# Optimization experiments

Hardware: AMD Instinct MI355X
Metric: run time of the kernel (lower is better)

## Reference

```python
import jax, jax.numpy as jnp
import numpy as np

# Swin block config (matches init_kwargs)
DIM = 192
HEADS = 6
HEAD_DIM = 32
INNER = HEADS * HEAD_DIM  # 192
MLP = 768
WS = 7                    # window size
DISP = WS // 2            # cyclic shift displacement = 3
NEG = -1e9                # stands in for -inf in the shift masks
EPS = 1e-5


def setup_inputs() -> dict:
    key = jax.random.key(0)
    ks = jax.random.split(key, 8)
    B, H, W = 8, 112, 112
    x = jax.random.normal(ks[0], (B, H, W, DIM), dtype=jnp.float32)
    w_qkv = jax.random.normal(ks[1], (DIM, 3 * INNER), dtype=jnp.float32) * 0.02
    w_out = jax.random.normal(ks[2], (INNER, DIM), dtype=jnp.float32) * 0.02
    b_out = jnp.zeros((DIM,), jnp.float32)
    pos_emb = jax.random.normal(ks[3], (2 * WS - 1, 2 * WS - 1), dtype=jnp.float32)
    ln1_g = jnp.ones((DIM,), jnp.float32)
    ln1_b = jnp.zeros((DIM,), jnp.float32)
    ln2_g = jnp.ones((DIM,), jnp.float32)
    ln2_b = jnp.zeros((DIM,), jnp.float32)
    w1 = jax.random.normal(ks[4], (DIM, MLP), dtype=jnp.float32) * 0.02
    b1 = jnp.zeros((MLP,), jnp.float32)
    w2 = jax.random.normal(ks[5], (MLP, DIM), dtype=jnp.float32) * 0.02
    b2 = jnp.zeros((DIM,), jnp.float32)
    return {"x": x, "w_qkv": w_qkv, "w_out": w_out, "b_out": b_out,
            "pos_emb": pos_emb, "ln1_g": ln1_g, "ln1_b": ln1_b,
            "ln2_g": ln2_g, "ln2_b": ln2_b,
            "w1": w1, "b1": b1, "w2": w2, "b2": b2}


def _layernorm(x, g, b):
    mu = jnp.mean(x, axis=-1, keepdims=True)
    var = jnp.var(x, axis=-1, keepdims=True)
    return (x - mu) * jax.lax.rsqrt(var + EPS) * g + b


def _rel_bias(pos_emb):
    # relative position bias, gathered to (ws^2, ws^2)
    coords = jnp.stack(jnp.meshgrid(jnp.arange(WS), jnp.arange(WS), indexing="ij"), -1).reshape(-1, 2)
    rel = coords[:, None, :] - coords[None, :, :] + WS - 1  # in [0, 2*WS-2]
    return pos_emb[rel[..., 0], rel[..., 1]]


def _shift_masks(nw_h, nw_w):
    ws2 = WS * WS
    ul = jnp.zeros((ws2, ws2), jnp.float32)
    ul = ul.at[-DISP * WS:, :-DISP * WS].set(NEG)
    ul = ul.at[:-DISP * WS, -DISP * WS:].set(NEG)
    lr = jnp.zeros((WS, WS, WS, WS), jnp.float32)
    lr = lr.at[:, -DISP:, :, :-DISP].set(NEG)
    lr = lr.at[:, :-DISP:, :, -DISP:].set(NEG)
    lr = lr.reshape(ws2, ws2)
    full = jnp.zeros((nw_h * nw_w, ws2, ws2), jnp.float32)
    full = full.at[-nw_w:].add(ul)            # bottom row of windows
    full = full.at[nw_w - 1::nw_w].add(lr)    # rightmost column of windows
    return full


def _window_attention(x, w_qkv, w_out, b_out, pos_emb):
    x = jnp.roll(x, (-DISP, -DISP), axis=(1, 2))  # cyclic shift
    B, H, W, _ = x.shape
    nw_h, nw_w = H // WS, W // WS
    ws2 = WS * WS
    qkv = x @ w_qkv  # (B,H,W,3*INNER)
    qkv = qkv.reshape(B, nw_h, WS, nw_w, WS, 3, HEADS, HEAD_DIM)
    # -> (3, B, heads, n_windows, ws^2, head_dim)
    qkv = qkv.transpose(5, 0, 6, 1, 3, 2, 4, 7).reshape(3, B, HEADS, nw_h * nw_w, ws2, HEAD_DIM)
    q, k, v = qkv[0], qkv[1], qkv[2]
    dots = jnp.einsum("bhwid,bhwjd->bhwij", q, k) * (HEAD_DIM ** -0.5)
    dots = dots + _rel_bias(pos_emb)                       # (ws2,ws2) broadcast
    dots = dots + _shift_masks(nw_h, nw_w)                 # (nw,ws2,ws2) broadcast
    attn = jax.nn.softmax(dots, axis=-1)
    out = jnp.einsum("bhwij,bhwjd->bhwid", attn, v)
    # merge windows back: (B, nw_h, WS, nw_w, WS, heads*head_dim)
    out = out.reshape(B, HEADS, nw_h, nw_w, WS, WS, HEAD_DIM)
    out = out.transpose(0, 2, 4, 3, 5, 1, 6).reshape(B, H, W, INNER)
    out = out @ w_out + b_out
    return jnp.roll(out, (DISP, DISP), axis=(1, 2))  # cyclic back-shift


def reference(x, w_qkv, w_out, b_out, pos_emb, ln1_g, ln1_b, ln2_g, ln2_b, w1, b1, w2, b2):
    # Residual(PreNorm(WindowAttention))
    x = x + _window_attention(_layernorm(x, ln1_g, ln1_b), w_qkv, w_out, b_out, pos_emb)
    # Residual(PreNorm(FeedForward))  with exact (erf) GELU as in nn.GELU
    h = _layernorm(x, ln2_g, ln2_b)
    h = jax.nn.gelu(h @ w1 + b1, approximate=False) @ w2 + b2
    return x + h
```

## Files before the change

kernel.cpp:

```cpp
#include <hip/hip_runtime.h>
#include <hip/hip_bf16.h>
#include <math.h>

typedef __hip_bfloat16 bf16;
typedef unsigned short ushort_t;
typedef __bf16 bf16x8 __attribute__((ext_vector_type(8)));
typedef unsigned short ushortx8 __attribute__((ext_vector_type(8)));
typedef float  f32x4  __attribute__((ext_vector_type(4)));

#define BATCH 8
#define HH 112
#define WW 112
#define CDIM 192
#define HEADS 6
#define HD 32
#define QKVW 576
#define MLPW 768
#define WS 7
#define WS2 49
#define NWH 16
#define NWW 16
#define NWIN 256
#define NTOK (BATCH*HH*WW)
#define NEGV (-1e9f)

typedef __attribute__((address_space(3))) void lds_void;
typedef const __attribute__((address_space(1))) void gbl_void;

__device__ __forceinline__ float toF(float v) { return v; }
__device__ __forceinline__ float toF(bf16 v) { return __bfloat162float(v); }
__device__ __forceinline__ bf16  f2b(float v) { return __float2bfloat16(v); }
__device__ __forceinline__ ushort_t f2u(float v) { bf16 b = __float2bfloat16(v); return *(ushort_t*)&b; }

__device__ __forceinline__ bool probe_is_bf16(const void* p) {
    const unsigned int* w = (const unsigned int*)p;
    int nz = 0, band = 0;
    #pragma unroll
    for (int i = 0; i < 16; i++) {
        unsigned int v = w[i];
        if (v == 0u) continue;
        nz++;
        unsigned int lo = v & 0xFFFFu, hi = v >> 16;
        unsigned int elo = (lo >> 7) & 0xFFu, ehi = (hi >> 7) & 0xFFu;
        bool okl = (lo != 0u) && (elo >= 0x60u) && (elo <= 0x9Fu);
        bool okh = (hi != 0u) && (ehi >= 0x60u) && (ehi <= 0x9Fu);
        if (okl && okh) band++;
    }
    return (nz == 0) || (band == nz);
}

__device__ __forceinline__ float read_any(const void* p, size_t i, bool isb) {
    return isb ? toF(((const bf16*)p)[i]) : ((const float*)p)[i];
}

__device__ __forceinline__ float wave_sum(float v) {
    #pragma unroll
    for (int o = 1; o < 64; o <<= 1) v += __shfl_xor(v, o, 64);
    return v;
}

__global__ void canon_small_kernel(const void* s0, const void* s1, const void* s2,
                                   const void* s3, const void* s4, const void* s5,
                                   const void* s6, const void* s7,
                                   float* __restrict__ cW) {
    const void* srcs[8] = {s0, s1, s2, s3, s4, s5, s6, s7};
    const int off[8]  = {0, 192, 361, 553, 745, 937, 1129, 1897};
    const int cnt[8]  = {192, 169, 192, 192, 192, 192, 768, 192};
    const int doff[8] = {0, 192, 384, 576, 768, 960, 1152, 1920};
    int i = blockIdx.x * 256 + threadIdx.x;
    if (i >= 2089) return;
    int s = 0;
    #pragma unroll
    for (int k = 1; k < 8; k++) if (i >= off[k]) s = k;
    int j = i - off[s];
    if (j < cnt[s]) {
        bool isb = probe_is_bf16(srcs[s]);
        cW[doff[s] + j] = read_any(srcs[s], j, isb);
    }
}

__global__ void canon_bt4_kernel(const void* w0, const void* w1, const void* w2,
                                 const void* w3, ushort_t* __restrict__ cT) {
    int bid = blockIdx.x;
    const void* src; ushort_t* dst; int K, N, base;
    if (bid < 432)       { src = w0; dst = cT;          K = CDIM; N = QKVW; base = bid; }
    else if (bid < 576)  { src = w1; dst = cT + 110592; K = CDIM; N = CDIM; base = bid - 432; }
    else if (bid < 1152) { src = w2; dst = cT + 147456; K = CDIM; N = MLPW; base = bid - 576; }
    else                 { src = w3; dst = cT + 294912; K = MLPW; N = CDIM; base = bid - 1152; }
    int i = base * 256 + threadIdx.x;
    if (i < K * N) {
        bool isb = probe_is_bf16(src);
        int k = i / N, n = i % N;
        dst[(size_t)n * K + k] = f2u(read_any(src, i, isb));
    }
}

__global__ void ln1_kernel(const void* __restrict__ xraw, const float* __restrict__ g,
                           const float* __restrict__ bta, bf16* __restrict__ out) {
    bool xb = probe_is_bf16(xraw);
    int wave = threadIdx.x >> 6, lane = threadIdx.x & 63;
    int t = blockIdx.x * 4 + wave;
    size_t base = (size_t)t * CDIM;
    float v[3];
    #pragma unroll
    for (int i = 0; i < 3; i++) v[i] = read_any(xraw, base + lane + 64 * i, xb);
    float s  = v[0] + v[1] + v[2];
    float s2 = v[0]*v[0] + v[1]*v[1] + v[2]*v[2];
    s = wave_sum(s); s2 = wave_sum(s2);
    float mu = s * (1.0f / CDIM);
    float var = s2 * (1.0f / CDIM) - mu * mu;
    float rs = rsqrtf(var + 1e-5f);
    #pragma unroll
    for (int i = 0; i < 3; i++) {
        int c = lane + 64 * i;
        out[base + c] = f2b((v[i] - mu) * rs * g[c] + bta[c]);
    }
}

template <int EPI, int NY>
__global__ __launch_bounds__(256) void gemm192_kernel(
    const ushort_t* __restrict__ A, const ushort_t* __restrict__ BT,
    const int N,
    const float* __restrict__ bias,
    const void* __restrict__ res,
    void* __restrict__ out)
{
    __shared__ ushort_t As[3][128 * 64];
    __shared__ ushort_t Bs[3][64 * 64];
    int tid = threadIdx.x;
    int per = gridDim.x >> 3;
    int sid = blockIdx.x;
    int w = (sid & 7) * per + (sid >> 3);
    int t0 = (w / NY) * 128;
    int n0 = (w % NY) * 64;
    int lane = tid & 63, wv = tid >> 6;
    int l15 = lane & 15, quad = lane >> 4;
    int lr = lane >> 3, lc = lane & 7;

    #pragma unroll
    for (int p = 0; p < 3; p++) {
        #pragma unroll
        for (int it = 0; it < 4; it++) {
            int r = wv * 32 + it * 8 + lr;
            const ushort_t* src = &A[(size_t)(t0 + r) * 192 + p * 64 + ((lc ^ lr) << 3)];
            __builtin_amdgcn_global_load_lds(
                (gbl_void*)src, (lds_void*)&As[p][(wv * 32 + it * 8) * 64], 16, 0, 0);
        }
        #pragma unroll
        for (int it = 0; it < 2; it++) {
            int r = wv * 16 + it * 8 + lr;
            const ushort_t* src = &BT[(size_t)(n0 + r) * 192 + p * 64 + ((lc ^ lr) << 3)];
            __builtin_amdgcn_global_load_lds(
                (gbl_void*)src, (lds_void*)&Bs[p][(wv * 16 + it * 8) * 64], 16, 0, 0);
        }
    }

    f32x4 acc[2][4];
    #pragma unroll
    for (int i = 0; i < 2; i++)
        #pragma unroll
        for (int j = 0; j < 4; j++)
            acc[i][j] = (f32x4){0.f, 0.f, 0.f, 0.f};

    __syncthreads();

    #pragma unroll
    for (int kk = 0; kk < 6; kk++) {
        int p = kk >> 1;
        int cs = ((((kk & 1) * 4 + quad)) ^ (l15 & 7)) << 3;
        bf16x8 af[2], bfr[4];
        #pragma unroll
        for (int i = 0; i < 2; i++)
            af[i] = *(const bf16x8*)(&As[p][(wv * 32 + i * 16 + l15) * 64 + cs]);
        #pragma unroll
        for (int j = 0; j < 4; j++)
            bfr[j] = *(const bf16x8*)(&Bs[p][(j * 16 + l15) * 64 + cs]);
        #pragma unroll
        for (int i = 0; i < 2; i++)
            #pragma unroll
            for (int j = 0; j < 4; j++)
                acc[i][j] = __builtin_amdgcn_mfma_f32_16x16x32_bf16(af[i], bfr[j], acc[i][j], 0, 0, 0);
    }

    bool xb = false;
    if (EPI == 1) xb = probe_is_bf16(res);

    #pragma unroll
    for (int i = 0; i < 2; i++) {
        #pragma unroll
        for (int j = 0; j < 4; j++) {
            #pragma unroll
            for (int r = 0; r < 4; r++) {
                int row = wv * 32 + i * 16 + quad * 4 + r;
                int col = n0 + j * 16 + l15;
                size_t t = (size_t)(t0 + row);
                float v = acc[i][j][r];
                if (EPI == 0) {
                    ((bf16*)out)[t * N + col] = f2b(v);
                } else {
                    size_t o = t * CDIM + col;
                    ((bf16*)out)[o] = f2b(v + bias[col] + read_any(res, o, xb));
                }
            }
        }
    }
}

__global__ __launch_bounds__(256, 2) void fused_mlp_kernel(
    const bf16* __restrict__ X,
    const ushort_t* __restrict__ W1T,
    const ushort_t* __restrict__ W2T,
    const float* __restrict__ g, const float* __restrict__ bta,
    const float* __restrict__ b1, const float* __restrict__ b2,
    float* __restrict__ out)
{
    __shared__ ushort_t W1s[3 * 64 * 64];
    __shared__ ushort_t W2s[192 * 64];
    __shared__ ushort_t Hs[128 * 64];
    int tid = threadIdx.x;
    int lane = tid & 63, wv = tid >> 6;
    int l15 = lane & 15, quad = lane >> 4;
    int lr = lane >> 3, lc = lane & 7;
    int t0 = blockIdx.x * 128;

    auto stageW1 = [&](int c) {
        #pragma unroll
        for (int p = 0; p < 3; p++)
            #pragma unroll
            for (int rg = 0; rg < 2; rg++) {
                int rowb = wv * 16 + rg * 8;
                const ushort_t* src =
                    &W1T[(size_t)(c * 64 + rowb + lr) * CDIM + p * 64 + ((lc ^ lr) << 3)];
                __builtin_amdgcn_global_load_lds(
                    (gbl_void*)src, (lds_void*)&W1s[p * 4096 + rowb * 64], 16, 0, 0);
            }
    };
    auto stageW2 = [&](int c) {
        #pragma unroll
        for (int rg = 0; rg < 6; rg++) {
            int rowb = wv * 48 + rg * 8;
            const ushort_t* src =
                &W2T[(size_t)(rowb + lr) * MLPW + c * 64 + ((lc ^ lr) << 3)];
            __builtin_amdgcn_global_load_lds(
                (gbl_void*)src, (lds_void*)&W2s[rowb * 64], 16, 0, 0);
        }
    };

    stageW1(0);
    stageW2(0);

    bf16x8 af[2][6];
    float s[2] = {0.f, 0.f}, s2[2] = {0.f, 0.f};
    #pragma unroll
    for (int m = 0; m < 2; m++) {
        size_t rb = (size_t)(t0 + wv * 32 + m * 16 + l15) * CDIM;
        #pragma unroll
        for (int kk = 0; kk < 6; kk++) {
            af[m][kk] = *(const bf16x8*)((const ushort_t*)X + rb + kk * 32 + quad * 8);
            #pragma unroll
            for (int j = 0; j < 8; j++) {
                float f = (float)af[m][kk][j];
                s[m] += f; s2[m] += f * f;
            }
        }
    }
    #pragma unroll
    for (int m = 0; m < 2; m++) {
        s[m]  += __shfl_xor(s[m], 16, 64);  s[m]  += __shfl_xor(s[m], 32, 64);
        s2[m] += __shfl_xor(s2[m], 16, 64); s2[m] += __shfl_xor(s2[m], 32, 64);
    }
    #pragma unroll
    for (int kk = 0; kk < 6; kk++) {
        int c0 = kk * 32 + quad * 8;
        float4 g0 = *(const float4*)(g + c0), g1 = *(const float4*)(g + c0 + 4);
        float4 b0 = *(const float4*)(bta + c0), b1v = *(const float4*)(bta + c0 + 4);
        const float* gp[2] = {&g0.x, &g1.x};
        const float* bp[2] = {&b0.x, &b1v.x};
        #pragma unroll
        for (int m = 0; m < 2; m++) {
            float mu = s[m] * (1.0f / CDIM);
            float var = s2[m] * (1.0f / CDIM) - mu * mu;
            float rs = rsqrtf(var + 1e-5f);
            #pragma unroll
            for (int j = 0; j < 8; j++)
                af[m][kk][j] = (__bf16)(((float)af[m][kk][j] - mu) * rs * gp[j >> 2][j & 3]
                                        + bp[j >> 2][j & 3]);
        }
    }

    f32x4 acc2[2][12];
    #pragma unroll
    for (int m = 0; m < 2; m++)
        #pragma unroll
        for (int nt = 0; nt < 12; nt++) acc2[m][nt] = (f32x4){0.f, 0.f, 0.f, 0.f};

    __syncthreads();

    for (int c = 0; c < 12; c++) {
        f32x4 hacc[2][4];
        #pragma unroll
        for (int m = 0; m < 2; m++)
            #pragma unroll
            for (int nt = 0; nt < 4; nt++) hacc[m][nt] = (f32x4){0.f, 0.f, 0.f, 0.f};
        #pragma unroll
        for (int kk = 0; kk < 6; kk++) {
            int p = kk >> 1;
            int cc = (kk & 1) * 4 + quad;
            #pragma unroll
            for (int nt = 0; nt < 4; nt++) {
                int n = nt * 16 + l15;
                bf16x8 bfr = *(const bf16x8*)(&W1s[p * 4096 + n * 64 + ((cc ^ (n & 7)) << 3)]);
                #pragma unroll
                for (int m = 0; m < 2; m++)
                    hacc[m][nt] = __builtin_amdgcn_mfma_f32_16x16x32_bf16(af[m][kk], bfr, hacc[m][nt], 0, 0, 0);
            }
        }
        float b1v[4];
        #pragma unroll
        for (int nt = 0; nt < 4; nt++) b1v[nt] = b1[c * 64 + nt * 16 + l15];
        #pragma unroll
        for (int m = 0; m < 2; m++) {
            #pragma unroll
            for (int nt = 0; nt < 4; nt++) {
                #pragma unroll
                for (int r = 0; r < 4; r++) {
                    int i = wv * 32 + m * 16 + quad * 4 + r;
                    int hcol = nt * 16 + l15;
                    float a = hacc[m][nt][r] + b1v[nt];
                    float yv = 0.7978845608028654f * (a + 0.044715f * a * a * a);
                    float th = 1.0f - 2.0f / (__expf(2.0f * yv) + 1.0f);
                    float gl = 0.5f * a * (1.0f + th);
                    Hs[i * 64 + (((hcol >> 3) ^ (i & 7)) << 3) + (hcol & 7)] = f2u(gl);
                }
            }
        }
        __syncthreads();

        if (c + 1 < 12) stageW1(c + 1);

        #pragma unroll
        for (int kt = 0; kt < 2; kt++) {
            int cc = kt * 4 + quad;
            bf16x8 pa[2];
            #pragma unroll
            for (int m = 0; m < 2; m++) {
                int row = wv * 32 + m * 16 + l15;
                pa[m] = *(const bf16x8*)(&Hs[row * 64 + ((cc ^ (row & 7)) << 3)]);
            }
            #pragma unroll
            for (int nt = 0; nt < 12; nt++) {
                int n = nt * 16 + l15;
                bf16x8 wb = *(const bf16x8*)(&W2s[n * 64 + ((cc ^ (n & 7)) << 3)]);
                #pragma unroll
                for (int m = 0; m < 2; m++)
                    acc2[m][nt] = __builtin_amdgcn_mfma_f32_16x16x32_bf16(pa[m], wb, acc2[m][nt], 0, 0, 0);
            }
        }
        __syncthreads();

        if (c + 1 < 12) stageW2(c + 1);
    }

    #pragma unroll
    for (int nt = 0; nt < 12; nt++) {
        float bb = b2[nt * 16 + l15];
        #pragma unroll
        for (int m = 0; m < 2; m++) {
            #pragma unroll
            for (int r = 0; r < 4; r++) {
                int row = t0 + wv * 32 + m * 16 + quad * 4 + r;
                int col = nt * 16 + l15;
                size_t o = (size_t)row * CDIM + col;
                out[o] = acc2[m][nt][r] + bb + toF(X[o]);
            }
        }
    }
}

__global__ __launch_bounds__(256) void attn_kernel(const bf16* __restrict__ qkv,
                                                   const float* __restrict__ pos_emb,
                                                   bf16* __restrict__ y) {
    __shared__ ushort_t Ps[4][64 * 72];
    __shared__ ushort_t Vt[4][32 * 72];
    __shared__ float pe[169];

    int tid = threadIdx.x;
    int wv = tid >> 6, lane = tid & 63;
    int l15 = lane & 15, quad = lane >> 4;

    int per = gridDim.x >> 3;
    int sid = blockIdx.x;
    int bid = (sid & 7) * per + (sid >> 3);
    int gid = bid * 4 + wv;
    int h = gid % HEADS;
    int rest = gid / HEADS;
    int win = rest % NWIN;
    int b = rest / NWIN;
    int wi = win >> 4, wj = win & 15;

    for (int i = lane; i < 169; i += 64) pe[i] = pos_emb[i];
    __syncthreads();

    auto tok = [&](int i) -> int {
        i = min(i, 48);
        int pi = (i * 37) >> 8;
        int pj = i - pi * 7;
        int ui = wi * WS + pi + 3; if (ui >= HH) ui -= HH;
        int uj = wj * WS + pj + 3; if (uj >= WW) uj -= WW;
        return (b * HH + ui) * WW + uj;
    };

    bf16x8 qf[4], kf[4];
    #pragma unroll
    for (int t = 0; t < 4; t++) {
        size_t base = (size_t)tok(t * 16 + l15) * QKVW + h * HD + quad * 8;
        qf[t] = *(const bf16x8*)(qkv + base);
        kf[t] = *(const bf16x8*)(qkv + base + CDIM);
    }

    #pragma unroll
    for (int it = 0; it < 4; it++) {
        int idx = lane + it * 64;
        int p = idx >> 2, dc = idx & 3;
        size_t base = (size_t)tok(p) * QKVW + 2 * CDIM + h * HD + dc * 8;
        ushortx8 v = *(const ushortx8*)((const ushort_t*)qkv + base);
        #pragma unroll
        for (int jj = 0; jj < 8; jj++)
            Vt[wv][(dc * 8 + jj) * 72 + p] = v[jj];
    }

    f32x4 acc[4][4];
    #pragma unroll
    for (int mt = 0; mt < 4; mt++)
        #pragma unroll
        for (int nt = 0; nt < 4; nt++)
            acc[mt][nt] = (f32x4){0.f, 0.f, 0.f, 0.f};
    #pragma unroll
    for (int mt = 0; mt < 4; mt++)
        #pragma unroll
        for (int nt = 0; nt < 4; nt++)
            acc[mt][nt] = __builtin_amdgcn_mfma_f32_16x16x32_bf16(qf[mt], kf[nt], acc[mt][nt], 0, 0, 0);

    bool m_ul = (wi == NWH - 1);
    bool m_lr = (wj == NWW - 1);
    int kpi[4], kpj[4];
    bool jval[4];
    #pragma unroll
    for (int nt = 0; nt < 4; nt++) {
        int j = nt * 16 + l15;
        jval[nt] = (j < WS2);
        int jc = min(j, 48);
        kpi[nt] = (jc * 37) >> 8;
        kpj[nt] = jc - kpi[nt] * 7;
    }
    #pragma unroll
    for (int mt = 0; mt < 4; mt++) {
        #pragma unroll
        for (int r = 0; r < 4; r++) {
            int i = mt * 16 + quad * 4 + r;
            int ic = min(i, 48);
            int pi = (ic * 37) >> 8;
            int pj = ic - pi * 7;
            #pragma unroll
            for (int nt = 0; nt < 4; nt++) {
                float s = acc[mt][nt][r] * 0.17677669529663689f
                        + pe[(pi - kpi[nt] + 6) * 13 + (pj - kpj[nt] + 6)];
                if (m_ul && ((pi >= 4) != (kpi[nt] >= 4))) s += NEGV;
                if (m_lr && ((pj >= 4) != (kpj[nt] >= 4))) s += NEGV;
                if (!jval[nt]) s = NEGV;
                acc[mt][nt][r] = s;
            }
            float mx = fmaxf(fmaxf(acc[mt][0][r], acc[mt][1][r]),
                             fmaxf(acc[mt][2][r], acc[mt][3][r]));
            #pragma unroll
            for (int o = 1; o < 16; o <<= 1) mx = fmaxf(mx, __shfl_xor(mx, o, 64));
            float sum = 0.f;
            #pragma unroll
            for (int nt = 0; nt < 4; nt++) {
                float e = __expf(acc[mt][nt][r] - mx);
                acc[mt][nt][r] = e;
                sum += e;
            }
            #pragma unroll
            for (int o = 1; o < 16; o <<= 1) sum += __shfl_xor(sum, o, 64);
            float inv = 1.0f / sum;
            #pragma unroll
            for (int nt = 0; nt < 4; nt++) acc[mt][nt][r] *= inv;
        }
    }

    #pragma unroll
    for (int mt = 0; mt < 4; mt++)
        #pragma unroll
        for (int nt = 0; nt < 4; nt++)
            #pragma unroll
            for (int r = 0; r < 4; r++)
                Ps[wv][(mt * 16 + quad * 4 + r) * 72 + nt * 16 + l15] = f2u(acc[mt][nt][r]);

    f32x4 oacc[4][2];
    #pragma unroll
    for (int mt = 0; mt < 4; mt++)
        #pragma unroll
        for (int nt = 0; nt < 2; nt++)
            oacc[mt][nt] = (f32x4){0.f, 0.f, 0.f, 0.f};
    #pragma unroll
    for (int kt = 0; kt < 2; kt++) {
        bf16x8 pa[4], vb[2];
        #pragma unroll
        for (int mt = 0; mt < 4; mt++)
            pa[mt] = *(const bf16x8*)(&Ps[wv][(mt * 16 + l15) * 72 + kt * 32 + quad * 8]);
        #pragma unroll
        for (int nt = 0; nt < 2; nt++)
            vb[nt] = *(const bf16x8*)(&Vt[wv][(nt * 16 + l15) * 72 + kt * 32 + quad * 8]);
        #pragma unroll
        for (int mt = 0; mt < 4; mt++)
            #pragma unroll
            for (int nt = 0; nt < 2; nt++)
                oacc[mt][nt] = __builtin_amdgcn_mfma_f32_16x16x32_bf16(pa[mt], vb[nt], oacc[mt][nt], 0, 0, 0);
    }

    #pragma unroll
    for (int mt = 0; mt < 4; mt++) {
        #pragma unroll
        for (int r = 0; r < 4; r++) {
            int i = mt * 16 + quad * 4 + r;
            if (i < WS2) {
                size_t base = (size_t)tok(i) * CDIM + h * HD + l15;
                #pragma unroll
                for (int nt = 0; nt < 2; nt++)
                    y[base + nt * 16] = f2b(oacc[mt][nt][r]);
            }
        }
    }
}

extern "C" void kernel_launch(void* const* d_in, const int* in_sizes, int n_in,
                              void* d_out, int out_size, void* d_ws, size_t ws_size,
                              hipStream_t stream) {
    float* out = (float*)d_out;

    size_t szA = (size_t)NTOK * CDIM * sizeof(bf16);
    size_t szQ = (size_t)NTOK * QKVW * sizeof(bf16);
    size_t szY = (size_t)NTOK * CDIM * sizeof(bf16);
    size_t szX = (size_t)NTOK * CDIM * sizeof(bf16);
    size_t szP = 3072 * sizeof(float);
    size_t szT = 442368 * sizeof(ushort_t);
    if (ws_size < szA + szQ + szY + szX + szP + szT) return;
    bf16*     bufA = (bf16*)d_ws;
    bf16*     bufQ = (bf16*)((char*)d_ws + szA);
    bf16*     bufY = (bf16*)((char*)d_ws + szA + szQ);
    bf16*     bufX = (bf16*)((char*)d_ws + szA + szQ + szY);
    float*    cW   = (float*)((char*)d_ws + szA + szQ + szY + szX);
    ushort_t* cT   = (ushort_t*)((char*)d_ws + szA + szQ + szY + szX + szP);

    float* cBout = cW + 0;
    float* cPe   = cW + 192;
    float* cL1g  = cW + 384;
    float* cL1b  = cW + 576;
    float* cL2g  = cW + 768;
    float* cL2b  = cW + 960;
    float* cB1   = cW + 1152;
    float* cB2   = cW + 1920;

    ushort_t* tWqkv = cT + 0;
    ushort_t* tWout = cT + 110592;
    ushort_t* tW1   = cT + 147456;
    ushort_t* tW2   = cT + 294912;

    dim3 b256(256);
    canon_small_kernel<<<9, b256, 0, stream>>>(
        d_in[3], d_in[4], d_in[5], d_in[6], d_in[7], d_in[8], d_in[10], d_in[12], cW);
    canon_bt4_kernel<<<1728, b256, 0, stream>>>(
        d_in[1], d_in[2], d_in[9], d_in[11], cT);

    int gLN = NTOK / 4;
    int gM  = NTOK / 128;
    int gAT = BATCH * NWIN * HEADS / 4;
    int gF  = NTOK / 128;

    ln1_kernel<<<gLN, b256, 0, stream>>>(d_in[0], cL1g, cL1b, bufA);
    gemm192_kernel<0, 9><<<gM * 9, b256, 0, stream>>>(
        (const ushort_t*)bufA, tWqkv, QKVW, nullptr, nullptr, bufQ);
    attn_kernel<<<gAT, b256, 0, stream>>>(bufQ, cPe, bufY);
    gemm192_kernel<1, 3><<<gM * 3, b256, 0, stream>>>(
        (const ushort_t*)bufY, tWout, CDIM, cBout, d_in[0], bufX);
    fused_mlp_kernel<<<gF, b256, 0, stream>>>(
        bufX, tW1, tW2, cL2g, cL2b, cB1, cB2, out);
}
```

Before: 508.8 us.

## Fuse LayerNorm1 into QKV GEMM and load A operand directly to registers

Result: slower. 526.3 us (+3.4%).

```diff
diff --git a/kernel.cpp b/kernel.cpp
--- a/kernel.cpp
+++ b/kernel.cpp
@@ -53,12 +53,6 @@
     return isb ? toF(((const bf16*)p)[i]) : ((const float*)p)[i];
 }
 
-__device__ __forceinline__ float wave_sum(float v) {
-    #pragma unroll
-    for (int o = 1; o < 64; o <<= 1) v += __shfl_xor(v, o, 64);
-    return v;
-}
-
 __global__ void canon_small_kernel(const void* s0, const void* s1, const void* s2,
                                    const void* s3, const void* s4, const void* s5,
                                    const void* s6, const void* s7,
@@ -95,37 +89,16 @@
     }
 }
 
-__global__ void ln1_kernel(const void* __restrict__ xraw, const float* __restrict__ g,
-                           const float* __restrict__ bta, bf16* __restrict__ out) {
-    bool xb = probe_is_bf16(xraw);
-    int wave = threadIdx.x >> 6, lane = threadIdx.x & 63;
-    int t = blockIdx.x * 4 + wave;
-    size_t base = (size_t)t * CDIM;
-    float v[3];
-    #pragma unroll
-    for (int i = 0; i < 3; i++) v[i] = read_any(xraw, base + lane + 64 * i, xb);
-    float s  = v[0] + v[1] + v[2];
-    float s2 = v[0]*v[0] + v[1]*v[1] + v[2]*v[2];
-    s = wave_sum(s); s2 = wave_sum(s2);
-    float mu = s * (1.0f / CDIM);
-    float var = s2 * (1.0f / CDIM) - mu * mu;
-    float rs = rsqrtf(var + 1e-5f);
-    #pragma unroll
-    for (int i = 0; i < 3; i++) {
-        int c = lane + 64 * i;
-        out[base + c] = f2b((v[i] - mu) * rs * g[c] + bta[c]);
-    }
-}
-
 template <int EPI, int NY>
-__global__ __launch_bounds__(256) void gemm192_kernel(
-    const ushort_t* __restrict__ A, const ushort_t* __restrict__ BT,
+__global__ __launch_bounds__(256) void gemm192f_kernel(
+    const void* __restrict__ Araw,
+    const ushort_t* __restrict__ BT,
     const int N,
+    const float* __restrict__ g, const float* __restrict__ bta,
     const float* __restrict__ bias,
     const void* __restrict__ res,
     void* __restrict__ out)
 {
-    __shared__ ushort_t As[3][128 * 64];
     __shared__ ushort_t Bs[3][64 * 64];
     int tid = threadIdx.x;
     int per = gridDim.x >> 3;
@@ -140,13 +113,6 @@
     #pragma unroll
     for (int p = 0; p < 3; p++) {
         #pragma unroll
-        for (int it = 0; it < 4; it++) {
-            int r = wv * 32 + it * 8 + lr;
-            const ushort_t* src = &A[(size_t)(t0 + r) * 192 + p * 64 + ((lc ^ lr) << 3)];
-            __builtin_amdgcn_global_load_lds(
-                (gbl_void*)src, (lds_void*)&As[p][(wv * 32 + it * 8) * 64], 16, 0, 0);
-        }
-        #pragma unroll
         for (int it = 0; it < 2; it++) {
             int r = wv * 16 + it * 8 + lr;
             const ushort_t* src = &BT[(size_t)(n0 + r) * 192 + p * 64 + ((lc ^ lr) << 3)];
@@ -155,6 +121,86 @@
         }
     }
 
+    bf16x8 af[2][6];
+    if (EPI == 0) {
+        bool xb = probe_is_bf16(Araw);
+        if (xb) {
+            const ushort_t* xh = (const ushort_t*)Araw;
+            #pragma unroll
+            for (int m = 0; m < 2; m++) {
+                size_t rb = (size_t)(t0 + wv * 32 + m * 16 + l15) * CDIM;
+                float s = 0.f, s2 = 0.f;
+                #pragma unroll
+                for (int kk = 0; kk < 6; kk++) {
+                    af[m][kk] = *(const bf16x8*)(xh + rb + kk * 32 + quad * 8);
+                    #pragma unroll
+                    for (int j = 0; j < 8; j++) {
+                        float f = (float)af[m][kk][j];
+                        s += f; s2 += f * f;
+                    }
+                }
+                s  += __shfl_xor(s, 16, 64);  s  += __shfl_xor(s, 32, 64);
+                s2 += __shfl_xor(s2, 16, 64); s2 += __shfl_xor(s2, 32, 64);
+                float mu = s * (1.0f / CDIM);
+                float rs = rsqrtf(s2 * (1.0f / CDIM) - mu * mu + 1e-5f);
+                #pragma unroll
+                for (int kk = 0; kk < 6; kk++) {
+                    int c0 = kk * 32 + quad * 8;
+                    float4 g0 = *(const float4*)(g + c0), g1 = *(const float4*)(g + c0 + 4);
+                    float4 b0 = *(const float4*)(bta + c0), b1v = *(const float4*)(bta + c0 + 4);
+                    const float* gp[2] = {&g0.x, &g1.x};
+                    const float* bp[2] = {&b0.x, &b1v.x};
+                    #pragma unroll
+                    for (int j = 0; j < 8; j++)
+                        af[m][kk][j] = (__bf16)(((float)af[m][kk][j] - mu) * rs * gp[j >> 2][j & 3]
+                                                + bp[j >> 2][j & 3]);
+                }
+            }
+        } else {
+            const float* xf = (const float*)Araw;
+            #pragma unroll
+            for (int m = 0; m < 2; m++) {
+                size_t rb = (size_t)(t0 + wv * 32 + m * 16 + l15) * CDIM;
+                float va[6][8];
+                float s = 0.f, s2 = 0.f;
+                #pragma unroll
+                for (int kk = 0; kk < 6; kk++) {
+                    float4 a0 = *(const float4*)(xf + rb + kk * 32 + quad * 8);
+                    float4 a1 = *(const float4*)(xf + rb + kk * 32 + quad * 8 + 4);
+                    va[kk][0] = a0.x; va[kk][1] = a0.y; va[kk][2] = a0.z; va[kk][3] = a0.w;
+                    va[kk][4] = a1.x; va[kk][5] = a1.y; va[kk][6] = a1.z; va[kk][7] = a1.w;
+                    #pragma unroll
+                    for (int j = 0; j < 8; j++) { s += va[kk][j]; s2 += va[kk][j] * va[kk][j]; }
+                }
+                s  += __shfl_xor(s, 16, 64);  s  += __shfl_xor(s, 32, 64);
+                s2 += __shfl_xor(s2, 16, 64); s2 += __shfl_xor(s2, 32, 64);
+                float mu = s * (1.0f / CDIM);
+                float rs = rsqrtf(s2 * (1.0f / CDIM) - mu * mu + 1e-5f);
+                #pragma unroll
+                for (int kk = 0; kk < 6; kk++) {
+                    int c0 = kk * 32 + quad * 8;
+                    float4 g0 = *(const float4*)(g + c0), g1 = *(const float4*)(g + c0 + 4);
+                    float4 b0 = *(const float4*)(bta + c0), b1v = *(const float4*)(bta + c0 + 4);
+                    const float* gp[2] = {&g0.x, &g1.x};
+                    const float* bp[2] = {&b0.x, &b1v.x};
+                    #pragma unroll
+                    for (int j = 0; j < 8; j++)
+                        af[m][kk][j] = (__bf16)((va[kk][j] - mu) * rs * gp[j >> 2][j & 3]
+                                                + bp[j >> 2][j & 3]);
+                }
+            }
+        }
+    } else {
+        const ushort_t* ah = (const ushort_t*)Araw;
+        #pragma unroll
+        for (int m = 0; m < 2; m++) {
+            size_t rb = (size_t)(t0 + wv * 32 + m * 16 + l15) * CDIM;
+            #pragma unroll
+            for (int kk = 0; kk < 6; kk++)
+                af[m][kk] = *(const bf16x8*)(ah + rb + kk * 32 + quad * 8);
+        }
+    }
+
     f32x4 acc[2][4];
     #pragma unroll
     for (int i = 0; i < 2; i++)
@@ -168,10 +214,7 @@
     for (int kk = 0; kk < 6; kk++) {
         int p = kk >> 1;
         int cs = ((((kk & 1) * 4 + quad)) ^ (l15 & 7)) << 3;
-        bf16x8 af[2], bfr[4];
-        #pragma unroll
-        for (int i = 0; i < 2; i++)
-            af[i] = *(const bf16x8*)(&As[p][(wv * 32 + i * 16 + l15) * 64 + cs]);
+        bf16x8 bfr[4];
         #pragma unroll
         for (int j = 0; j < 4; j++)
             bfr[j] = *(const bf16x8*)(&Bs[p][(j * 16 + l15) * 64 + cs]);
@@ -179,7 +222,7 @@
         for (int i = 0; i < 2; i++)
             #pragma unroll
             for (int j = 0; j < 4; j++)
-                acc[i][j] = __builtin_amdgcn_mfma_f32_16x16x32_bf16(af[i], bfr[j], acc[i][j], 0, 0, 0);
+                acc[i][j] = __builtin_amdgcn_mfma_f32_16x16x32_bf16(af[i][kk], bfr[j], acc[i][j], 0, 0, 0);
     }
 
     bool xb = false;
@@ -546,7 +589,6 @@
     size_t szP = 3072 * sizeof(float);
     size_t szT = 442368 * sizeof(ushort_t);
     if (ws_size < szA + szQ + szY + szX + szP + szT) return;
-    bf16*     bufA = (bf16*)d_ws;
     bf16*     bufQ = (bf16*)((char*)d_ws + szA);
     bf16*     bufY = (bf16*)((char*)d_ws + szA + szQ);
     bf16*     bufX = (bf16*)((char*)d_ws + szA + szQ + szY);
@@ -573,17 +615,15 @@
     canon_bt4_kernel<<<1728, b256, 0, stream>>>(
         d_in[1], d_in[2], d_in[9], d_in[11], cT);
 
-    int gLN = NTOK / 4;
     int gM  = NTOK / 128;
     int gAT = BATCH * NWIN * HEADS / 4;
     int gF  = NTOK / 128;
 
-    ln1_kernel<<<gLN, b256, 0, stream>>>(d_in[0], cL1g, cL1b, bufA);
-    gemm192_kernel<0, 9><<<gM * 9, b256, 0, stream>>>(
-        (const ushort_t*)bufA, tWqkv, QKVW, nullptr, nullptr, bufQ);
+    gemm192f_kernel<0, 9><<<gM * 9, b256, 0, stream>>>(
+        d_in[0], tWqkv, QKVW, cL1g, cL1b, nullptr, nullptr, bufQ);
     attn_kernel<<<gAT, b256, 0, stream>>>(bufQ, cPe, bufY);
-    gemm192_kernel<1, 3><<<gM * 3, b256, 0, stream>>>(
-        (const ushort_t*)bufY, tWout, CDIM, cBout, d_in[0], bufX);
+    gemm192f_kernel<1, 3><<<gM * 3, b256, 0, stream>>>(
+        bufY, tWout, CDIM, nullptr, nullptr, cBout, d_in[0], bufX);
     fused_mlp_kernel<<<gF, b256, 0, stream>>>(
         bufX, tW1, tW2, cL2g, cL2b, cB1, cB2, out);
 }
```

## Load GEMM A operand directly into registers; transpose attention PV for packed stores

Applied to the files above, without the earlier changes.

Result: no change. 510.5 us (+0.3%).

```diff
diff --git a/kernel.cpp b/kernel.cpp
--- a/kernel.cpp
+++ b/kernel.cpp
@@ -118,14 +118,14 @@
 }
 
 template <int EPI, int NY>
-__global__ __launch_bounds__(256) void gemm192_kernel(
-    const ushort_t* __restrict__ A, const ushort_t* __restrict__ BT,
+__global__ __launch_bounds__(256) void gemm192r_kernel(
+    const ushort_t* __restrict__ A,
+    const ushort_t* __restrict__ BT,
     const int N,
     const float* __restrict__ bias,
     const void* __restrict__ res,
     void* __restrict__ out)
 {
-    __shared__ ushort_t As[3][128 * 64];
     __shared__ ushort_t Bs[3][64 * 64];
     int tid = threadIdx.x;
     int per = gridDim.x >> 3;
@@ -140,13 +140,6 @@
     #pragma unroll
     for (int p = 0; p < 3; p++) {
         #pragma unroll
-        for (int it = 0; it < 4; it++) {
-            int r = wv * 32 + it * 8 + lr;
-            const ushort_t* src = &A[(size_t)(t0 + r) * 192 + p * 64 + ((lc ^ lr) << 3)];
-            __builtin_amdgcn_global_load_lds(
-                (gbl_void*)src, (lds_void*)&As[p][(wv * 32 + it * 8) * 64], 16, 0, 0);
-        }
-        #pragma unroll
         for (int it = 0; it < 2; it++) {
             int r = wv * 16 + it * 8 + lr;
             const ushort_t* src = &BT[(size_t)(n0 + r) * 192 + p * 64 + ((lc ^ lr) << 3)];
@@ -155,6 +148,15 @@
         }
     }
 
+    bf16x8 af[2][6];
+    #pragma unroll
+    for (int m = 0; m < 2; m++) {
+        size_t rb = (size_t)(t0 + wv * 32 + m * 16 + l15) * CDIM;
+        #pragma unroll
+        for (int kk = 0; kk < 6; kk++)
+            af[m][kk] = *(const bf16x8*)(A + rb + kk * 32 + quad * 8);
+    }
+
     f32x4 acc[2][4];
     #pragma unroll
     for (int i = 0; i < 2; i++)
@@ -168,10 +170,7 @@
     for (int kk = 0; kk < 6; kk++) {
         int p = kk >> 1;
         int cs = ((((kk & 1) * 4 + quad)) ^ (l15 & 7)) << 3;
-        bf16x8 af[2], bfr[4];
-        #pragma unroll
-        for (int i = 0; i < 2; i++)
-            af[i] = *(const bf16x8*)(&As[p][(wv * 32 + i * 16 + l15) * 64 + cs]);
+        bf16x8 bfr[4];
         #pragma unroll
         for (int j = 0; j < 4; j++)
             bfr[j] = *(const bf16x8*)(&Bs[p][(j * 16 + l15) * 64 + cs]);
@@ -179,7 +178,7 @@
         for (int i = 0; i < 2; i++)
             #pragma unroll
             for (int j = 0; j < 4; j++)
-                acc[i][j] = __builtin_amdgcn_mfma_f32_16x16x32_bf16(af[i], bfr[j], acc[i][j], 0, 0, 0);
+                acc[i][j] = __builtin_amdgcn_mfma_f32_16x16x32_bf16(af[i][kk], bfr[j], acc[i][j], 0, 0, 0);
     }
 
     bool xb = false;
@@ -497,38 +496,40 @@
             for (int r = 0; r < 4; r++)
                 Ps[wv][(mt * 16 + quad * 4 + r) * 72 + nt * 16 + l15] = f2u(acc[mt][nt][r]);
 
-    f32x4 oacc[4][2];
-    #pragma unroll
-    for (int mt = 0; mt < 4; mt++)
-        #pragma unroll
-        for (int nt = 0; nt < 2; nt++)
-            oacc[mt][nt] = (f32x4){0.f, 0.f, 0.f, 0.f};
+    f32x4 oaccT[2][4];
+    #pragma unroll
+    for (int dt = 0; dt < 2; dt++)
+        #pragma unroll
+        for (int it = 0; it < 4; it++)
+            oaccT[dt][it] = (f32x4){0.f, 0.f, 0.f, 0.f};
     #pragma unroll
     for (int kt = 0; kt < 2; kt++) {
         bf16x8 pa[4], vb[2];
         #pragma unroll
-        for (int mt = 0; mt < 4; mt++)
-            pa[mt] = *(const bf16x8*)(&Ps[wv][(mt * 16 + l15) * 72 + kt * 32 + quad * 8]);
-        #pragma unroll
-        for (int nt = 0; nt < 2; nt++)
-            vb[nt] = *(const bf16x8*)(&Vt[wv][(nt * 16 + l15) * 72 + kt * 32 + quad * 8]);
-        #pragma unroll
-        for (int mt = 0; mt < 4; mt++)
-            #pragma unroll
-            for (int nt = 0; nt < 2; nt++)
-                oacc[mt][nt] = __builtin_amdgcn_mfma_f32_16x16x32_bf16(pa[mt], vb[nt], oacc[mt][nt], 0, 0, 0);
-    }
-
-    #pragma unroll
-    for (int mt = 0; mt < 4; mt++) {
-        #pragma unroll
-        for (int r = 0; r < 4; r++) {
-            int i = mt * 16 + quad * 4 + r;
-            if (i < WS2) {
-                size_t base = (size_t)tok(i) * CDIM + h * HD + l15;
-                #pragma unroll
-                for (int nt = 0; nt < 2; nt++)
-                    y[base + nt * 16] = f2b(oacc[mt][nt][r]);
+        for (int it = 0; it < 4; it++)
+            pa[it] = *(const bf16x8*)(&Ps[wv][(it * 16 + l15) * 72 + kt * 32 + quad * 8]);
+        #pragma unroll
+        for (int dt = 0; dt < 2; dt++)
+            vb[dt] = *(const bf16x8*)(&Vt[wv][(dt * 16 + l15) * 72 + kt * 32 + quad * 8]);
+        #pragma unroll
+        for (int dt = 0; dt < 2; dt++)
+            #pragma unroll
+            for (int it = 0; it < 4; it++)
+                oaccT[dt][it] = __builtin_amdgcn_mfma_f32_16x16x32_bf16(vb[dt], pa[it], oaccT[dt][it], 0, 0, 0);
+    }
+
+    #pragma unroll
+    for (int it = 0; it < 4; it++) {
+        int i = it * 16 + l15;
+        if (i < WS2) {
+            size_t base = (size_t)tok(i) * CDIM + h * HD + quad * 4;
+            #pragma unroll
+            for (int dt = 0; dt < 2; dt++) {
+                unsigned int u0 = (unsigned int)f2u(oaccT[dt][it][0])
+                                | ((unsigned int)f2u(oaccT[dt][it][1]) << 16);
+                unsigned int u1 = (unsigned int)f2u(oaccT[dt][it][2])
+                                | ((unsigned int)f2u(oaccT[dt][it][3]) << 16);
+                *(uint2*)((ushort_t*)y + base + dt * 16) = make_uint2(u0, u1);
             }
         }
     }
@@ -579,10 +580,10 @@
     int gF  = NTOK / 128;
 
     ln1_kernel<<<gLN, b256, 0, stream>>>(d_in[0], cL1g, cL1b, bufA);
-    gemm192_kernel<0, 9><<<gM * 9, b256, 0, stream>>>(
+    gemm192r_kernel<0, 9><<<gM * 9, b256, 0, stream>>>(
         (const ushort_t*)bufA, tWqkv, QKVW, nullptr, nullptr, bufQ);
     attn_kernel<<<gAT, b256, 0, stream>>>(bufQ, cPe, bufY);
-    gemm192_kernel<1, 3><<<gM * 3, b256, 0, stream>>>(
+    gemm192r_kernel<1, 3><<<gM * 3, b256, 0, stream>>>(
         (const ushort_t*)bufY, tWout, CDIM, cBout, d_in[0], bufX);
     fused_mlp_kernel<<<gF, b256, 0, stream>>>(
         bufX, tW1, tW2, cL2g, cL2b, cB1, cB2, out);
```
